# Optimization experiments

Measured on AMD Instinct MI355X. Metric: run time of the kernel, lower is better.

Reference implementation:

```python
import jax, jax.numpy as jnp
import numpy as np

EMBED = 1024
HEADS = 16
HEAD_DIM = EMBED // HEADS


def setup_inputs() -> dict:
    key = jax.random.key(0)
    ks = jax.random.split(key, 7)
    s = 1.0 / np.sqrt(EMBED)
    return {
        "hidden_states": jax.random.normal(ks[0], (8, 1024, EMBED), dtype=jnp.float32),
        "w_q": jax.random.uniform(ks[1], (EMBED, EMBED), jnp.float32, -s, s),
        "b_q": jax.random.uniform(ks[2], (EMBED,), jnp.float32, -s, s),
        "w_k": jax.random.uniform(ks[3], (EMBED, EMBED), jnp.float32, -s, s),
        "b_k": jax.random.uniform(ks[4], (EMBED,), jnp.float32, -s, s),
        "w_v": jax.random.uniform(ks[5], (EMBED, EMBED), jnp.float32, -s, s),
        "b_v": jax.random.uniform(ks[6], (EMBED,), jnp.float32, -s, s),
    }


def reference(hidden_states, w_q, b_q, w_k, b_k, w_v, b_v):
    b, L, c = hidden_states.shape
    h, d = HEADS, HEAD_DIM
    # torch Linear: x @ W.T + b
    q = hidden_states @ w_q.T + b_q
    k = hidden_states @ w_k.T + b_k
    v = hidden_states @ w_v.T + b_v
    # [b, L, h, d] -> [b, h, L, d]
    q = q.reshape(b, L, h, d).transpose(0, 2, 1, 3)
    k = k.reshape(b, L, h, d).transpose(0, 2, 1, 3)
    v = v.reshape(b, L, h, d).transpose(0, 2, 1, 3)
    scores = jnp.einsum("bhqd,bhkd->bhqk", q, k) * (d ** -0.5)
    probs = jax.nn.softmax(scores, axis=-1)
    out = jnp.einsum("bhqk,bhkd->bhqd", probs, v)  # [b, h, L, d]
    # Faithful to original: .view(b, L, -1) on [b,h,L,d] WITHOUT head transpose
    return out.reshape(b, L, h * d)
```

## Files before the change

kernel.cpp:

```cpp
#include <hip/hip_runtime.h>

#define EMBED 1024
#define HEADS 16
#define HDIM  64

typedef __attribute__((ext_vector_type(8))) short bf16x8;
typedef __attribute__((ext_vector_type(8))) _Float16 f16x8;
typedef __attribute__((ext_vector_type(4))) float f32x4;

#define AS1 __attribute__((address_space(1)))
#define AS3 __attribute__((address_space(3)))

#if __has_builtin(__builtin_amdgcn_exp2f)
#define EXP2F(x) __builtin_amdgcn_exp2f(x)
#else
#define EXP2F(x) exp2f(x)
#endif

__device__ __forceinline__ unsigned bf16_rne(float f) {
    unsigned u = __float_as_uint(f);
    return (u + 0x7FFFu + ((u >> 16) & 1u)) >> 16;
}

__global__ __launch_bounds__(256)
void cast_all(const float* __restrict__ X,  const float* __restrict__ Wq,
              const float* __restrict__ Wk, const float* __restrict__ Wv,
              short* __restrict__ Xh, short* __restrict__ Wh)
{
    const int bid = blockIdx.x;
    const float* in;
    short* out;
    float scale;
    int base;
    if (bid < 4096) { in = X; out = Xh; scale = 1.0f; base = bid; }
    else {
        const int wsel = (bid - 4096) >> 9;
        in  = (wsel == 0) ? Wq : (wsel == 1) ? Wk : Wv;
        out = Wh + wsel * 1048576;
        scale = 256.0f;
        base = (bid - 4096) & 511;
    }
    const int i = (base * 256 + threadIdx.x) * 8;
    float4 a = *(const float4*)(in + i);
    float4 b = *(const float4*)(in + i + 4);
    float f[8] = {a.x, a.y, a.z, a.w, b.x, b.y, b.z, b.w};
    union { _Float16 h[8]; uint4 v; } H;
#pragma unroll
    for (int e = 0; e < 8; ++e) H.h[e] = (_Float16)(f[e] * scale);
    *(uint4*)(out + i) = H.v;
}

#define STAGE_A(buf, h, kt) do {                                              \
    const short* s0_ = baseA + ((h) * 128) * EMBED + (kt) * 64;               \
    short* d_ = &sh[(buf) * 32768 + (h) * 8192 + t * 8];                      \
    __builtin_amdgcn_global_load_lds((const AS1 void*)s0_, (AS3 void*)d_, 16, 0, 0); \
    __builtin_amdgcn_global_load_lds((const AS1 void*)(s0_ + 64 * EMBED), (AS3 void*)(d_ + 4096), 16, 0, 0); \
} while (0)

#define STAGE_B(buf, h, kt) do {                                              \
    const short* s0_ = baseB + ((h) * 32) * EMBED + (kt) * 64;                \
    short* d_ = &sh[(buf) * 32768 + 16384 + (h) * 8192 + t * 8];              \
    __builtin_amdgcn_global_load_lds((const AS1 void*)s0_, (AS3 void*)d_, 16, 0, 0); \
    __builtin_amdgcn_global_load_lds((const AS1 void*)(s0_ + 128 * EMBED), (AS3 void*)(d_ + 4096), 16, 0, 0); \
} while (0)

__global__ __launch_bounds__(512, 2)
void qkv_mfma(const short* __restrict__ Xh, const short* __restrict__ Wh,
              const float* __restrict__ bq, const float* __restrict__ bk,
              const float* __restrict__ bv,
              short* __restrict__ Qb, short* __restrict__ Kb, short* __restrict__ Vn)
{
    __shared__ short sh[65536];

    const int t = threadIdx.x;
    const int lane = t & 63, quad = lane >> 4, l16 = lane & 15;
    const int w = t >> 6, wm = w >> 2, wn = w & 3;

    const int n0 = blockIdx.x * 256;
    const int m0 = blockIdx.y * 256;

    const int r  = t >> 3;
    const int k8 = ((t & 7) ^ (r & 7)) * 8;
    const short* baseA = Xh + (size_t)(m0 + r) * EMBED + k8;
    const short* baseB = Wh + (size_t)(n0 + (r & 31) + (r >> 5) * 64) * EMBED + k8;

    const int xk0 = ((quad * 16)      ^ ((l16 & 7) << 4)) >> 1;
    const int xk1 = ((64 + quad * 16) ^ ((l16 & 7) << 4)) >> 1;
    const int aOff = wm * 8192 + l16 * 64;
    const int bOff = 16384 + wn * 2048 + l16 * 64;

    f32x4 acc[8][4];
#pragma unroll
    for (int i = 0; i < 8; ++i)
#pragma unroll
        for (int j = 0; j < 4; ++j) acc[i][j] = (f32x4){0.f, 0.f, 0.f, 0.f};

    STAGE_B(0, 0, 0);
    STAGE_A(0, 0, 0);
    STAGE_A(0, 1, 0);
    STAGE_B(0, 1, 0);
    asm volatile("s_waitcnt vmcnt(4)" ::: "memory");
    __builtin_amdgcn_s_barrier();

#pragma unroll 1
    for (int i = 0; i < 8; ++i) {
        const int ktb = 2 * i + 1;
        const int ktc = 2 * i + 2;
        const bool more = (i < 7);
#pragma unroll
        for (int p = 0; p < 8; ++p) {
            const int q = p & 3, buf = p >> 2;
            const int miH = (q & 1) * 4, niH = (q >> 1) * 2;

            f16x8 af[4][2], bf[2][2];
#pragma unroll
            for (int mi = 0; mi < 4; ++mi) {
                const int o = buf * 32768 + aOff + (miH + mi) * 1024;
                af[mi][0] = *(const f16x8*)&sh[o + xk0];
                af[mi][1] = *(const f16x8*)&sh[o + xk1];
            }
#pragma unroll
            for (int ni = 0; ni < 2; ++ni) {
                const int nig = niH + ni;
                const int o = buf * 32768 + bOff + (nig & 1) * 1024 + (nig >> 1) * 8192;
                bf[ni][0] = *(const f16x8*)&sh[o + xk0];
                bf[ni][1] = *(const f16x8*)&sh[o + xk1];
            }

            if      (p == 0) STAGE_B(1, 0, ktb);
            else if (p == 1) STAGE_A(1, 0, ktb);
            else if (p == 2) STAGE_A(1, 1, ktb);
            else if (p == 3) STAGE_B(1, 1, ktb);
            else if (more) {
                if      (p == 4) STAGE_B(0, 0, ktc);
                else if (p == 5) STAGE_A(0, 0, ktc);
                else if (p == 6) STAGE_A(0, 1, ktc);
                else             STAGE_B(0, 1, ktc);
            }

            if (p < 4 || more) asm volatile("s_waitcnt vmcnt(4)" ::: "memory");
            else if (p == 4)   asm volatile("s_waitcnt vmcnt(0)" ::: "memory");
            else               asm volatile("" ::: "memory");
            __builtin_amdgcn_s_barrier();

            __builtin_amdgcn_s_setprio(1);
#pragma unroll
            for (int mi = 0; mi < 4; ++mi)
#pragma unroll
                for (int ni = 0; ni < 2; ++ni) {
                    acc[miH + mi][niH + ni] = __builtin_amdgcn_mfma_f32_16x16x32_f16(
                        af[mi][0], bf[ni][0], acc[miH + mi][niH + ni], 0, 0, 0);
                    acc[miH + mi][niH + ni] = __builtin_amdgcn_mfma_f32_16x16x32_f16(
                        af[mi][1], bf[ni][1], acc[miH + mi][niH + ni], 0, 0, 0);
                }
            __builtin_amdgcn_s_setprio(0);
            __builtin_amdgcn_s_barrier();
        }
    }

    const int mat = n0 >> 10;
    const float* bias = (mat == 0) ? bq : (mat == 1) ? bk : bv;
    short* Out = (mat == 0) ? Qb : (mat == 1) ? Kb : Vn;
    const float s = (mat == 0) ? 0.125f * 1.4426950408889634f : 1.0f;
    const float fs = s * (1.0f / 256.0f);
    const int nm0 = n0 & 1023;
    float bias_v[4];
#pragma unroll
    for (int ni = 0; ni < 4; ++ni) bias_v[ni] = bias[nm0 + wn * 64 + ni * 16 + l16] * s;
    const int bidx = m0 >> 10;
    const int l0   = m0 & 1023;

#pragma unroll
    for (int mi = 0; mi < 8; ++mi) {
        __syncthreads();
#pragma unroll
        for (int ni = 0; ni < 4; ++ni) {
            const int col = wn * 64 + ni * 16 + l16;
#pragma unroll
            for (int rr = 0; rr < 4; ++rr) {
                const int srow = wm * 16 + quad * 4 + rr;
                sh[srow * 268 + col] =
                    (short)(unsigned short)bf16_rne(fmaf(acc[mi][ni][rr], fs, bias_v[ni]));
            }
        }
        __syncthreads();
        const int srw = t >> 4;
        const int c0  = (t & 15) * 16;
        uint4 v0 = *(uint4*)&sh[srw * 268 + c0];
        uint4 v1 = *(uint4*)&sh[srw * 268 + c0 + 8];
        const int wmS = srw >> 4, rloc = srw & 15;
        const int l = l0 + wmS * 128 + mi * 16 + rloc;
        const int nm = nm0 + c0;
        const int head = nm >> 6, d0 = nm & 63;
        short* pDst = Out + ((size_t)(bidx * HEADS + head) * 1024 + l) * 64 + d0;
        *(uint4*)pDst = v0;
        *(uint4*)(pDst + 8) = v1;
    }
}

__global__ __launch_bounds__(256)
void vtrans(const short* __restrict__ Vn, short* __restrict__ Vt)
{
    __shared__ int tile[64 * 65];
    const int t  = threadIdx.x;
    const int lt = blockIdx.x;
    const int bh = blockIdx.y;
    const int lq = t >> 3, dc = (t & 7) * 8;
    const short* src = Vn + ((size_t)bh * 1024 + lt * 64) * 64;
#pragma unroll
    for (int h = 0; h < 2; ++h) {
        const int l = lq + h * 32;
        union { uint4 v; unsigned short us[8]; } ld;
        ld.v = *(const uint4*)&src[l * 64 + dc];
#pragma unroll
        for (int j = 0; j < 8; ++j) tile[(dc + j) * 65 + l] = ld.us[j];
    }
    __syncthreads();
    const int dr = t >> 3, lblk = (t & 7) * 8;
    short* dst = Vt + (size_t)bh * 64 * 1024 + lt * 64;
#pragma unroll
    for (int h = 0; h < 2; ++h) {
        const int d = dr + h * 32;
        union { uint4 v; unsigned short us[8]; } o;
#pragma unroll
        for (int j = 0; j < 8; ++j) o.us[j] = (unsigned short)tile[d * 65 + lblk + j];
        *(uint4*)&dst[(size_t)d * 1024 + lblk] = o.v;
    }
}

__global__ __launch_bounds__(256)
void attn_mfma(const short* __restrict__ Qb, const short* __restrict__ Kb,
               const short* __restrict__ Vt, float* __restrict__ out)
{
    __shared__ short smem[25088];

    const int t  = threadIdx.x;
    const int id  = blockIdx.x;
    const int xcd = id & 7;
    const int loc = id >> 3;
    const int bh  = xcd * 16 + (loc >> 3);
    const int qt  = loc & 7;
    const int lane = t & 63, quad = lane >> 4, l16 = lane & 15;
    const int w = t >> 6;
    const int srow = t & 63, schunk = t >> 6;

    const int prow = ((srow >> 4) & 1) * 32 + ((srow >> 2) & 3) * 8
                   + (srow >> 5) * 4 + (srow & 3);

    {
#pragma unroll
        for (int u = 0; u < 2; ++u) {
            const short* gq = Qb + ((size_t)bh * 1024 + qt * 128 + u * 64 + srow) * 64 + schunk * 8;
            __builtin_amdgcn_global_load_lds((const AS1 void*)gq,        (AS3 void*)&smem[16384 + u * 4096 + t * 8],         16, 0, 0);
            __builtin_amdgcn_global_load_lds((const AS1 void*)(gq + 32), (AS3 void*)&smem[16384 + u * 4096 + (t + 256) * 8], 16, 0, 0);
        }
        const short* gk = Kb + ((size_t)bh * 1024 + prow) * 64 + schunk * 8;
        __builtin_amdgcn_global_load_lds((const AS1 void*)gk,        (AS3 void*)&smem[t * 8],         16, 0, 0);
        __builtin_amdgcn_global_load_lds((const AS1 void*)(gk + 32), (AS3 void*)&smem[(t + 256) * 8], 16, 0, 0);
        const short* gv = Vt + ((size_t)bh * 64 + srow) * 1024 + schunk * 8;
        __builtin_amdgcn_global_load_lds((const AS1 void*)gv,        (AS3 void*)&smem[8192 + t * 8],         16, 0, 0);
        __builtin_amdgcn_global_load_lds((const AS1 void*)(gv + 32), (AS3 void*)&smem[8192 + (t + 256) * 8], 16, 0, 0);
    }
    __syncthreads();

    bf16x8 qfrag[2][2];
#pragma unroll
    for (int u = 0; u < 2; ++u)
#pragma unroll
        for (int kh = 0; kh < 2; ++kh)
            qfrag[u][kh] = *(const bf16x8*)&smem[16384 + u * 4096 + ((quad + 4 * kh) * 64 + w * 16 + l16) * 8];

    f32x4 O[2][4];
#pragma unroll
    for (int u = 0; u < 2; ++u)
#pragma unroll
        for (int i = 0; i < 4; ++i) O[u][i] = (f32x4){0.f, 0.f, 0.f, 0.f};
    float l_i[2] = {0.f, 0.f};

    for (int kt = 0; kt < 16; ++kt) {
        const int cur = kt & 1, nxt = cur ^ 1;
        if (kt < 15) {
            const short* gk = Kb + ((size_t)bh * 1024 + (kt + 1) * 64 + prow) * 64 + schunk * 8;
            __builtin_amdgcn_global_load_lds((const AS1 void*)gk,        (AS3 void*)&smem[nxt * 4096 + t * 8],         16, 0, 0);
            __builtin_amdgcn_global_load_lds((const AS1 void*)(gk + 32), (AS3 void*)&smem[nxt * 4096 + (t + 256) * 8], 16, 0, 0);
            const short* gv = Vt + ((size_t)bh * 64 + srow) * 1024 + (kt + 1) * 64 + schunk * 8;
            __builtin_amdgcn_global_load_lds((const AS1 void*)gv,        (AS3 void*)&smem[8192 + nxt * 4096 + t * 8],         16, 0, 0);
            __builtin_amdgcn_global_load_lds((const AS1 void*)(gv + 32), (AS3 void*)&smem[8192 + nxt * 4096 + (t + 256) * 8], 16, 0, 0);
        }

        const short* Kc = &smem[cur * 4096];
        const short* Vc = &smem[8192 + cur * 4096];

#pragma unroll
        for (int u = 0; u < 2; ++u) {
            f32x4 ST[4];
#pragma unroll
            for (int mi = 0; mi < 4; ++mi) ST[mi] = (f32x4){0.f, 0.f, 0.f, 0.f};
            __builtin_amdgcn_s_setprio(1);
#pragma unroll
            for (int kh = 0; kh < 2; ++kh)
#pragma unroll
                for (int mi = 0; mi < 4; ++mi) {
                    const bf16x8 ka = *(const bf16x8*)&Kc[((quad + 4 * kh) * 64 + mi * 16 + l16) * 8];
                    ST[mi] = __builtin_amdgcn_mfma_f32_16x16x32_bf16(ka, qfrag[u][kh], ST[mi], 0, 0, 0);
                }
            __builtin_amdgcn_s_setprio(0);

            float p[4][4];
            float rs = 0.f;
#pragma unroll
            for (int mi = 0; mi < 4; ++mi)
#pragma unroll
                for (int rr = 0; rr < 4; ++rr) { p[mi][rr] = EXP2F(ST[mi][rr]); rs += p[mi][rr]; }
            l_i[u] += rs;

            union { unsigned uu[4]; bf16x8 v; } pa[2];
#pragma unroll
            for (int kh = 0; kh < 2; ++kh) {
                asm("v_cvt_pk_bf16_f32 %0, %1, %2" : "=v"(pa[kh].uu[0]) : "v"(p[kh][0]),     "v"(p[kh][1]));
                asm("v_cvt_pk_bf16_f32 %0, %1, %2" : "=v"(pa[kh].uu[1]) : "v"(p[kh][2]),     "v"(p[kh][3]));
                asm("v_cvt_pk_bf16_f32 %0, %1, %2" : "=v"(pa[kh].uu[2]) : "v"(p[kh + 2][0]), "v"(p[kh + 2][1]));
                asm("v_cvt_pk_bf16_f32 %0, %1, %2" : "=v"(pa[kh].uu[3]) : "v"(p[kh + 2][2]), "v"(p[kh + 2][3]));
            }

            __builtin_amdgcn_s_setprio(1);
#pragma unroll
            for (int kh = 0; kh < 2; ++kh)
#pragma unroll
                for (int mi = 0; mi < 4; ++mi) {
                    const bf16x8 va = *(const bf16x8*)&Vc[((quad + 4 * kh) * 64 + mi * 16 + l16) * 8];
                    O[u][mi] = __builtin_amdgcn_mfma_f32_16x16x32_bf16(va, pa[kh].v, O[u][mi], 0, 0, 0);
                }
            __builtin_amdgcn_s_setprio(0);
        }

        __syncthreads();
    }

#pragma unroll
    for (int u = 0; u < 2; ++u) {
        l_i[u] += __shfl_xor(l_i[u], 16);
        l_i[u] += __shfl_xor(l_i[u], 32);
    }

    float* Os = (float*)&smem[16384];
#pragma unroll
    for (int u = 0; u < 2; ++u) {
        __syncthreads();
        const float inv = 1.0f / l_i[u];
#pragma unroll
        for (int mi = 0; mi < 4; ++mi) {
            f32x4 v;
#pragma unroll
            for (int rr = 0; rr < 4; ++rr) v[rr] = O[u][mi][rr] * inv;
            *(f32x4*)&Os[(w * 16 + l16) * 68 + mi * 16 + quad * 4] = v;
        }
        __syncthreads();
        const int q = t >> 2, dbase = (t & 3) * 16;
        float* op = out + ((size_t)bh * 1024 + qt * 128 + u * 64 + q) * 64 + dbase;
#pragma unroll
        for (int i = 0; i < 4; ++i)
            *(float4*)&op[i * 4] = *(float4*)&Os[q * 68 + dbase + i * 4];
    }
}

extern "C" void kernel_launch(void* const* d_in, const int* in_sizes, int n_in,
                              void* d_out, int out_size, void* d_ws, size_t ws_size,
                              hipStream_t stream)
{
    const float* X  = (const float*)d_in[0];
    const float* Wq = (const float*)d_in[1];
    const float* bq = (const float*)d_in[2];
    const float* Wk = (const float*)d_in[3];
    const float* bk = (const float*)d_in[4];
    const float* Wv = (const float*)d_in[5];
    const float* bv = (const float*)d_in[6];
    float* out = (float*)d_out;

    const size_t per = (size_t)8 * HEADS * 1024 * HDIM;
    short* Qb = (short*)d_ws;
    short* Kb = Qb + per;
    short* Vt = Kb + per;
    short* Xh = Vt + per;
    short* Wh = Xh + per;
    short* Vn = (short*)d_out;

    cast_all<<<4096 + 3 * 512, 256, 0, stream>>>(X, Wq, Wk, Wv, Xh, Wh);

    qkv_mfma<<<dim3(12, 32), 512, 0, stream>>>(Xh, Wh, bq, bk, bv, Qb, Kb, Vn);
    vtrans<<<dim3(16, 128), 256, 0, stream>>>(Vn, Vt);
    attn_mfma<<<1024, 256, 0, stream>>>(Qb, Kb, Vt, out);
}
```

Before: 228.9 us.

## Fuse V transpose into QKV epilogue and double attention query tile per block

The QKV GEMM epilogue now writes the V projection directly in transposed [b,h,d,L] layout through a shared-memory transpose, so the separate vtrans kernel and its extra global round-trip and launch go away. The attention kernel now handles 256 queries per block instead of 128, launched as 512 blocks, so each K/V tile loaded into LDS serves more queries. The cost is more registers per thread (four O accumulators) and larger LDS, with launch bounds asking for two blocks per CU, plus fewer blocks in flight.

```diff
diff --git a/kernel.cpp b/kernel.cpp
--- a/kernel.cpp
+++ b/kernel.cpp
@@ -68,7 +68,7 @@
 void qkv_mfma(const short* __restrict__ Xh, const short* __restrict__ Wh,
               const float* __restrict__ bq, const float* __restrict__ bk,
               const float* __restrict__ bv,
-              short* __restrict__ Qb, short* __restrict__ Kb, short* __restrict__ Vn)
+              short* __restrict__ Qb, short* __restrict__ Kb, short* __restrict__ Vt)
 {
     __shared__ short sh[65536];
 
@@ -160,7 +160,6 @@
 
     const int mat = n0 >> 10;
     const float* bias = (mat == 0) ? bq : (mat == 1) ? bk : bv;
-    short* Out = (mat == 0) ? Qb : (mat == 1) ? Kb : Vn;
     const float s = (mat == 0) ? 0.125f * 1.4426950408889634f : 1.0f;
     const float fs = s * (1.0f / 256.0f);
     const int nm0 = n0 & 1023;
@@ -170,6 +169,35 @@
     const int bidx = m0 >> 10;
     const int l0   = m0 & 1023;
 
+    if (mat == 2) {
+#pragma unroll
+        for (int mi = 0; mi < 8; ++mi) {
+            __syncthreads();
+#pragma unroll
+            for (int ni = 0; ni < 4; ++ni) {
+                const int col = wn * 64 + ni * 16 + l16;
+                union { unsigned short us[4]; uint2 v; } pk;
+#pragma unroll
+                for (int rr = 0; rr < 4; ++rr)
+                    pk.us[rr] = (unsigned short)bf16_rne(fmaf(acc[mi][ni][rr], fs, bias_v[ni]));
+                *(uint2*)&sh[col * 40 + wm * 16 + quad * 4] = pk.v;
+            }
+            __syncthreads();
+            const int nm  = t & 255;
+            const int wmS = t >> 8;
+            uint4 v0 = *(uint4*)&sh[nm * 40 + wmS * 16];
+            uint4 v1 = *(uint4*)&sh[nm * 40 + wmS * 16 + 8];
+            const int nmg = nm0 + nm;
+            const int head = nmg >> 6, d0v = nmg & 63;
+            const int l = l0 + wmS * 128 + mi * 16;
+            short* pDst = Vt + ((size_t)(bidx * HEADS + head) * 64 + d0v) * 1024 + l;
+            *(uint4*)pDst = v0;
+            *(uint4*)(pDst + 8) = v1;
+        }
+        return;
+    }
+
+    short* Out = (mat == 0) ? Qb : Kb;
 #pragma unroll
     for (int mi = 0; mi < 8; ++mi) {
         __syncthreads();
@@ -198,48 +226,18 @@
     }
 }
 
-__global__ __launch_bounds__(256)
-void vtrans(const short* __restrict__ Vn, short* __restrict__ Vt)
-{
-    __shared__ int tile[64 * 65];
-    const int t  = threadIdx.x;
-    const int lt = blockIdx.x;
-    const int bh = blockIdx.y;
-    const int lq = t >> 3, dc = (t & 7) * 8;
-    const short* src = Vn + ((size_t)bh * 1024 + lt * 64) * 64;
-#pragma unroll
-    for (int h = 0; h < 2; ++h) {
-        const int l = lq + h * 32;
-        union { uint4 v; unsigned short us[8]; } ld;
-        ld.v = *(const uint4*)&src[l * 64 + dc];
-#pragma unroll
-        for (int j = 0; j < 8; ++j) tile[(dc + j) * 65 + l] = ld.us[j];
-    }
-    __syncthreads();
-    const int dr = t >> 3, lblk = (t & 7) * 8;
-    short* dst = Vt + (size_t)bh * 64 * 1024 + lt * 64;
-#pragma unroll
-    for (int h = 0; h < 2; ++h) {
-        const int d = dr + h * 32;
-        union { uint4 v; unsigned short us[8]; } o;
-#pragma unroll
-        for (int j = 0; j < 8; ++j) o.us[j] = (unsigned short)tile[d * 65 + lblk + j];
-        *(uint4*)&dst[(size_t)d * 1024 + lblk] = o.v;
-    }
-}
-
-__global__ __launch_bounds__(256)
+__global__ __launch_bounds__(256, 2)
 void attn_mfma(const short* __restrict__ Qb, const short* __restrict__ Kb,
                const short* __restrict__ Vt, float* __restrict__ out)
 {
-    __shared__ short smem[25088];
+    __shared__ short smem[32768];
 
     const int t  = threadIdx.x;
     const int id  = blockIdx.x;
     const int xcd = id & 7;
     const int loc = id >> 3;
-    const int bh  = xcd * 16 + (loc >> 3);
-    const int qt  = loc & 7;
+    const int bh  = xcd * 16 + (loc >> 2);
+    const int qt  = loc & 3;
     const int lane = t & 63, quad = lane >> 4, l16 = lane & 15;
     const int w = t >> 6;
     const int srow = t & 63, schunk = t >> 6;
@@ -249,8 +247,8 @@
 
     {
 #pragma unroll
-        for (int u = 0; u < 2; ++u) {
-            const short* gq = Qb + ((size_t)bh * 1024 + qt * 128 + u * 64 + srow) * 64 + schunk * 8;
+        for (int u = 0; u < 4; ++u) {
+            const short* gq = Qb + ((size_t)bh * 1024 + qt * 256 + u * 64 + srow) * 64 + schunk * 8;
             __builtin_amdgcn_global_load_lds((const AS1 void*)gq,        (AS3 void*)&smem[16384 + u * 4096 + t * 8],         16, 0, 0);
             __builtin_amdgcn_global_load_lds((const AS1 void*)(gq + 32), (AS3 void*)&smem[16384 + u * 4096 + (t + 256) * 8], 16, 0, 0);
         }
@@ -263,19 +261,19 @@
     }
     __syncthreads();
 
-    bf16x8 qfrag[2][2];
-#pragma unroll
-    for (int u = 0; u < 2; ++u)
+    bf16x8 qfrag[4][2];
+#pragma unroll
+    for (int u = 0; u < 4; ++u)
 #pragma unroll
         for (int kh = 0; kh < 2; ++kh)
             qfrag[u][kh] = *(const bf16x8*)&smem[16384 + u * 4096 + ((quad + 4 * kh) * 64 + w * 16 + l16) * 8];
 
-    f32x4 O[2][4];
-#pragma unroll
-    for (int u = 0; u < 2; ++u)
+    f32x4 O[4][4];
+#pragma unroll
+    for (int u = 0; u < 4; ++u)
 #pragma unroll
         for (int i = 0; i < 4; ++i) O[u][i] = (f32x4){0.f, 0.f, 0.f, 0.f};
-    float l_i[2] = {0.f, 0.f};
+    float l_i[4] = {0.f, 0.f, 0.f, 0.f};
 
     for (int kt = 0; kt < 16; ++kt) {
         const int cur = kt & 1, nxt = cur ^ 1;
@@ -292,7 +290,7 @@
         const short* Vc = &smem[8192 + cur * 4096];
 
 #pragma unroll
-        for (int u = 0; u < 2; ++u) {
+        for (int u = 0; u < 4; ++u) {
             f32x4 ST[4];
 #pragma unroll
             for (int mi = 0; mi < 4; ++mi) ST[mi] = (f32x4){0.f, 0.f, 0.f, 0.f};
@@ -338,14 +336,14 @@
     }
 
 #pragma unroll
-    for (int u = 0; u < 2; ++u) {
+    for (int u = 0; u < 4; ++u) {
         l_i[u] += __shfl_xor(l_i[u], 16);
         l_i[u] += __shfl_xor(l_i[u], 32);
     }
 
     float* Os = (float*)&smem[16384];
 #pragma unroll
-    for (int u = 0; u < 2; ++u) {
+    for (int u = 0; u < 4; ++u) {
         __syncthreads();
         const float inv = 1.0f / l_i[u];
 #pragma unroll
@@ -357,7 +355,7 @@
         }
         __syncthreads();
         const int q = t >> 2, dbase = (t & 3) * 16;
-        float* op = out + ((size_t)bh * 1024 + qt * 128 + u * 64 + q) * 64 + dbase;
+        float* op = out + ((size_t)bh * 1024 + qt * 256 + u * 64 + q) * 64 + dbase;
 #pragma unroll
         for (int i = 0; i < 4; ++i)
             *(float4*)&op[i * 4] = *(float4*)&Os[q * 68 + dbase + i * 4];
@@ -383,11 +381,9 @@
     short* Vt = Kb + per;
     short* Xh = Vt + per;
     short* Wh = Xh + per;
-    short* Vn = (short*)d_out;
 
     cast_all<<<4096 + 3 * 512, 256, 0, stream>>>(X, Wq, Wk, Wv, Xh, Wh);
 
-    qkv_mfma<<<dim3(12, 32), 512, 0, stream>>>(Xh, Wh, bq, bk, bv, Qb, Kb, Vn);
-    vtrans<<<dim3(16, 128), 256, 0, stream>>>(Vn, Vt);
-    attn_mfma<<<1024, 256, 0, stream>>>(Qb, Kb, Vt, out);
-}
+    qkv_mfma<<<dim3(12, 32), 512, 0, stream>>>(Xh, Wh, bq, bk, bv, Qb, Kb, Vt);
+    attn_mfma<<<512, 256, 0, stream>>>(Qb, Kb, Vt, out);
+}
```

After: 214.8 us. -6.1%, faster.
